# Kernel tuning notes

Hardware: AMD Instinct MI355X
Metric: run time of the kernel (lower is better)

The kernel has to match this reference:

```python
import jax, jax.numpy as jnp
import numpy as np

NUMERICAL_STABILIZER = 1e-3


def relu_kernel(data, projection_matrix):
    # data: [B,L,H,D], projection_matrix: [M,D] -> [B,L,H,M]
    ratio = 1.0 / jnp.sqrt(jnp.asarray(projection_matrix.shape[0], dtype=data.dtype))
    data_dash = ratio * jnp.einsum('blhd,md->blhm', data, projection_matrix)
    return jax.nn.relu(data_dash) + NUMERICAL_STABILIZER


def favor_causal(query, key, value, projection_matrix):
    # query/key/value: [B,L,H,D]; projection_matrix: [M,D]
    qp = relu_kernel(query, projection_matrix)  # [B,L,H,M]
    kp = relu_kernel(key, projection_matrix)    # [B,L,H,M]
    # move L to scan axis: [L,B,H,*]
    qs = jnp.transpose(qp, (1, 0, 2, 3))
    ks = jnp.transpose(kp, (1, 0, 2, 3))
    vs = jnp.transpose(value, (1, 0, 2, 3))

    B, H, M = qs.shape[1], qs.shape[2], qs.shape[3]
    D = vs.shape[3]
    kv0 = jnp.zeros((B, H, M, D), dtype=qs.dtype)
    ksum0 = jnp.zeros((B, H, M), dtype=qs.dtype)

    def step(carry, inp):
        kv_sum, k_sum = carry
        q_t, k_t, v_t = inp  # [B,H,M], [B,H,M], [B,H,D]
        kv_sum = kv_sum + jnp.einsum('bhm,bhd->bhmd', k_t, v_t)
        k_sum = k_sum + k_t
        num_t = jnp.einsum('bhmd,bhm->bhd', kv_sum, q_t)  # [B,H,D]
        den_t = jnp.einsum('bhm,bhm->bh', q_t, k_sum)     # [B,H]
        return (kv_sum, k_sum), (num_t, den_t)

    _, (num, den) = jax.lax.scan(step, (kv0, ksum0), (qs, ks, vs))
    # num: [L,B,H,D], den: [L,B,H]
    out = num / den[..., None]
    return jnp.transpose(out, (1, 0, 2, 3))  # [B,L,H,D]


def setup_inputs() -> dict:
    key = jax.random.key(0)
    k1, k2, k3, k4 = jax.random.split(key, 4)
    B, L, H, D, M = 2, 4096, 8, 64, 128
    return {
        'query': jax.random.normal(k1, (B, L, H, D), dtype=jnp.float32),
        'key': jax.random.normal(k2, (B, L, H, D), dtype=jnp.float32),
        'value': jax.random.normal(k3, (B, L, H, D), dtype=jnp.float32),
        'projection_matrix': jax.random.normal(k4, (M, D), dtype=jnp.float32),
    }


def reference(query, key, value, projection_matrix):
    return favor_causal(query, key, value, projection_matrix)
```

## Files before the change

### kernel.cpp

```cpp
#include <hip/hip_runtime.h>


#define B_ 2
#define L_ 4096
#define H_ 8
#define D_ 64
#define M_ 128
#define BH_ 16
#define HD_ 512
#define LHD_ (L_*HD_)
#define C_ 64
#define T_ 64
#define RATIO 0.08838834764831845f
#define EPS 1e-3f

#define REC_CS 8320
#define REC_F  8192
#define QF_OFF 8519680
#define N2_OFF 16908288
#define RS_OFF 25296896
#define P_OFF  25427968

#define SWZ64(r,c)  ((r)*64  + ((c) ^ (((r)&7)*8)))
#define SWZ128(r,c) ((r)*128 + ((c) ^ (((r)&15)*8)))

typedef __attribute__((ext_vector_type(8))) short bf16x8;
typedef __attribute__((ext_vector_type(4))) short bf16x4;
typedef __attribute__((ext_vector_type(4))) float f32x4;

__device__ __forceinline__ short f2bf(float f) {
  union { float f; unsigned u; } x; x.f = f;
  unsigned r = (x.u + 0x7fffu + ((x.u >> 16) & 1u)) >> 16;
  return (short)r;
}
__device__ __forceinline__ float bf2f(short s) {
  union { unsigned u; float f; } x; x.u = ((unsigned)(unsigned short)s) << 16;
  return x.f;
}
__device__ __forceinline__ bf16x8 cvt8(float4 a, float4 b) {
  union { bf16x8 v; short s[8]; } u;
  u.s[0]=f2bf(a.x); u.s[1]=f2bf(a.y); u.s[2]=f2bf(a.z); u.s[3]=f2bf(a.w);
  u.s[4]=f2bf(b.x); u.s[5]=f2bf(b.y); u.s[6]=f2bf(b.z); u.s[7]=f2bf(b.w);
  return u.v;
}
#define MFMA(a,b,c) __builtin_amdgcn_mfma_f32_16x16x32_bf16((a),(b),(c),0,0,0)

__global__ __launch_bounds__(256) void k0(
    const float* __restrict__ P, unsigned short* __restrict__ ws)
{
  const int i = (blockIdx.x*256 + threadIdx.x)*4;
  float4 p4 = *(const float4*)(P + i);
  union { bf16x4 v; short s[4]; } u;
  u.s[0]=f2bf(p4.x); u.s[1]=f2bf(p4.y); u.s[2]=f2bf(p4.z); u.s[3]=f2bf(p4.w);
  *(bf16x4*)(ws + P_OFF + i) = u.v;
}

__global__ __launch_bounds__(256) void k1(
    const float* __restrict__ qq, const float* __restrict__ kk,
    const float* __restrict__ vv, unsigned short* __restrict__ ws)
{
  __shared__ short Vt[64*64];
  __shared__ short Kft[128*64];
  __shared__ short KfTM[64*128];

  const int tid = threadIdx.x, bid = blockIdx.x;
  const int bh = bid >> 6, c = bid & 63;
  const int b = bh >> 3, h = bh & 7;
  const int lane = tid & 63, w = tid >> 6, quad = lane >> 4, l15 = lane & 15;
  const size_t gbase = (size_t)b*LHD_ + (size_t)h*D_;
  const int t0 = c*T_;
  const int trow = 16*w + l15;
  const unsigned short* Pb = ws + P_OFF;

  const float* qrow = qq + gbase + (size_t)(t0 + trow)*HD_;
  const float* krow = kk + gbase + (size_t)(t0 + trow)*HD_;
  float4 q4a = *(const float4*)(qrow + quad*8);
  float4 q4b = *(const float4*)(qrow + quad*8 + 4);
  float4 q4c = *(const float4*)(qrow + 32 + quad*8);
  float4 q4d = *(const float4*)(qrow + 32 + quad*8 + 4);
  float4 k4a = *(const float4*)(krow + quad*8);
  float4 k4b = *(const float4*)(krow + quad*8 + 4);
  float4 k4c = *(const float4*)(krow + 32 + quad*8);
  float4 k4d = *(const float4*)(krow + 32 + quad*8 + 4);

  for (int fi = tid; fi < 64*16; fi += 256) {
    int t = fi >> 4, d4 = (fi & 15)*4;
    float4 v4 = *(const float4*)(vv + gbase + (size_t)(t0+t)*HD_ + d4);
    Vt[SWZ64(d4+0, t)] = f2bf(v4.x);
    Vt[SWZ64(d4+1, t)] = f2bf(v4.y);
    Vt[SWZ64(d4+2, t)] = f2bf(v4.z);
    Vt[SWZ64(d4+3, t)] = f2bf(v4.w);
  }

  bf16x8 bq0 = cvt8(q4a, q4b), bq1 = cvt8(q4c, q4d);
  bf16x8 bk0 = cvt8(k4a, k4b), bk1 = cvt8(k4c, k4d);

  unsigned short* qfb = ws + QF_OFF + (size_t)(bh*C_+c)*REC_F;
  unsigned short* csb = ws + (size_t)(bh*C_+c)*REC_CS;

  bf16x4 qreg[8];
  #pragma unroll
  for (int ct = 0; ct < 8; ++ct) {
    bf16x8 ap0 = *(const bf16x8*)(Pb + (ct*16 + l15)*64 + quad*8);
    bf16x8 ap1 = *(const bf16x8*)(Pb + (ct*16 + l15)*64 + 32 + quad*8);
    f32x4 qa = {0.f,0.f,0.f,0.f}, ka = {0.f,0.f,0.f,0.f};
    qa = MFMA(ap0,bq0,qa); qa = MFMA(ap1,bq1,qa);
    ka = MFMA(ap0,bk0,ka); ka = MFMA(ap1,bk1,ka);
    union { bf16x4 v; short s[4]; } pq, pk;
    #pragma unroll
    for (int reg = 0; reg < 4; ++reg) {
      int m = 16*ct + 4*quad + reg;
      short qv = f2bf(fmaxf(qa[reg]*RATIO, 0.f) + EPS);
      short kv = f2bf(fmaxf(ka[reg]*RATIO, 0.f) + EPS);
      pq.s[reg] = qv; pk.s[reg] = kv;
      Kft[SWZ64(m, trow)] = kv;
    }
    qreg[ct] = pq.v;
    *(bf16x4*)(qfb + trow*128 + 16*ct + 4*quad) = pq.v;
    *(bf16x4*)&KfTM[SWZ128(trow, 16*ct + 4*quad)] = pk.v;
  }

  bf16x8 qfr[4];
  {
    const int src_lo = (2*(quad & 1))*16 + l15;
    #pragma unroll
    for (int ks2 = 0; ks2 < 4; ++ks2) {
      union { bf16x4 v; long long l; } a0, a1;
      a0.v = qreg[2*ks2]; a1.v = qreg[2*ks2+1];
      long long loA = __shfl(a0.l, src_lo, 64);
      long long hiA = __shfl(a0.l, src_lo + 16, 64);
      long long loB = __shfl(a1.l, src_lo, 64);
      long long hiB = __shfl(a1.l, src_lo + 16, 64);
      union { bf16x8 v8; long long l[2]; } r;
      r.l[0] = (quad < 2) ? loA : loB;
      r.l[1] = (quad < 2) ? hiA : hiB;
      qfr[ks2] = r.v8;
    }
  }
  __syncthreads();

  if (tid < 128) {
    float s = 0.f;
    #pragma unroll
    for (int i = 0; i < 8; ++i) {
      bf16x8 r = *(const bf16x8*)&Kft[SWZ64(tid, 8*i)];
      #pragma unroll
      for (int j = 0; j < 8; ++j) s += bf2f(r[j]);
    }
    csb[64*128 + tid] = (unsigned short)f2bf(s);
  }

  {
    bf16x8 av0 = *(const bf16x8*)&Vt[SWZ64(trow, 8*quad)];
    bf16x8 av1 = *(const bf16x8*)&Vt[SWZ64(trow, 32 + 8*quad)];
    #pragma unroll
    for (int mt = 0; mt < 8; ++mt) {
      bf16x8 b0 = *(const bf16x8*)&Kft[SWZ64(16*mt + l15, 8*quad)];
      bf16x8 b1 = *(const bf16x8*)&Kft[SWZ64(16*mt + l15, 32 + 8*quad)];
      f32x4 acc = {0.f,0.f,0.f,0.f};
      acc = MFMA(b0, av0, acc);
      acc = MFMA(b1, av1, acc);
      union { bf16x4 v; short s[4]; } pc;
      #pragma unroll
      for (int reg = 0; reg < 4; ++reg) pc.s[reg] = f2bf(acc[reg]);
      *(bf16x4*)(csb + trow*128 + 16*mt + 4*quad) = pc.v;
    }
  }

  f32x4 sacc[4];
  #pragma unroll
  for (int jt = 0; jt < 4; ++jt) { f32x4 z = {0.f,0.f,0.f,0.f}; sacc[jt] = z; }
  #pragma unroll
  for (int ks2 = 0; ks2 < 4; ++ks2) {
    #pragma unroll
    for (int jt = 0; jt < 4; ++jt) {
      bf16x8 bb = *(const bf16x8*)&KfTM[SWZ128(16*jt + l15, 32*ks2 + 8*quad)];
      sacc[jt] = MFMA(qfr[ks2], bb, sacc[jt]);
    }
  }
  __syncthreads();

  short* Sm = Kft;
  float rs[4] = {0.f,0.f,0.f,0.f};
  #pragma unroll
  for (int jt = 0; jt < 4; ++jt)
    #pragma unroll
    for (int reg = 0; reg < 4; ++reg) {
      int row = 16*w + 4*quad + reg;
      int j = l15 + 16*jt;
      float val = (j <= row) ? sacc[jt][reg] : 0.f;
      rs[reg] += val;
      Sm[SWZ64(row, j)] = f2bf(val);
    }
  #pragma unroll
  for (int reg = 0; reg < 4; ++reg) {
    rs[reg] += __shfl_xor(rs[reg], 1);
    rs[reg] += __shfl_xor(rs[reg], 2);
    rs[reg] += __shfl_xor(rs[reg], 4);
    rs[reg] += __shfl_xor(rs[reg], 8);
  }
  float* rsg = (float*)(ws + RS_OFF);
  if (l15 < 4) {
    float v = (l15==0) ? rs[0] : (l15==1) ? rs[1] : (l15==2) ? rs[2] : rs[3];
    rsg[bh*L_ + t0 + 16*w + 4*quad + l15] = v;
  }

  float* n2 = (float*)(ws + N2_OFF);
  f32x4 nacc[4];
  #pragma unroll
  for (int ct = 0; ct < 4; ++ct) { f32x4 z = {0.f,0.f,0.f,0.f}; nacc[ct] = z; }
  #pragma unroll
  for (int kss = 0; kss < 2; ++kss) {
    bf16x8 sb = *(const bf16x8*)&Sm[SWZ64(trow, 32*kss + 8*quad)];
    #pragma unroll
    for (int ct = 0; ct < 4; ++ct) {
      bf16x8 a = *(const bf16x8*)&Vt[SWZ64(16*ct + l15, 32*kss + 8*quad)];
      nacc[ct] = MFMA(a, sb, nacc[ct]);
    }
  }
  const int tg = t0 + trow;
  #pragma unroll
  for (int ct = 0; ct < 4; ++ct) {
    float4 o;
    o.x = nacc[ct][0]; o.y = nacc[ct][1]; o.z = nacc[ct][2]; o.w = nacc[ct][3];
    *(float4*)(n2 + gbase + (size_t)tg*HD_ + 16*ct + 4*quad) = o;
  }
}

__global__ __launch_bounds__(64) void k2(unsigned short* __restrict__ ws)
{
  const int gid = blockIdx.x*64 + threadIdx.x;
  const int bh = gid / 2080, e = (gid % 2080)*4;
  unsigned short* base = ws + (size_t)bh*C_*REC_CS + e;
  bf16x4 v[64];
  #pragma unroll
  for (int c2 = 0; c2 < 64; ++c2) v[c2] = *(const bf16x4*)(base + (size_t)c2*REC_CS);
  float run[4] = {0.f,0.f,0.f,0.f};
  #pragma unroll
  for (int c2 = 0; c2 < 64; ++c2) {
    union { bf16x4 v; short s[4]; } wv;
    #pragma unroll
    for (int j = 0; j < 4; ++j) { wv.s[j] = f2bf(run[j]); run[j] += bf2f(v[c2][j]); }
    *(bf16x4*)(base + (size_t)c2*REC_CS) = wv.v;
  }
}

__global__ __launch_bounds__(256) void k3(
    const unsigned short* __restrict__ ws, float* __restrict__ out)
{
  __shared__ short csL[64*128];
  __shared__ float ks_lds[128];

  const int tid = threadIdx.x, bid = blockIdx.x;
  const int bh = bid >> 6, c = bid & 63;
  const int b = bh >> 3, h = bh & 7;
  const int lane = tid & 63, w = tid >> 6, quad = lane >> 4, l15 = lane & 15;
  const size_t gbase = (size_t)b*LHD_ + (size_t)h*D_;
  const int t0 = c*T_;
  const unsigned short* csb = ws + (size_t)(bh*C_+c)*REC_CS;
  const unsigned short* qfb = ws + QF_OFF + (size_t)(bh*C_+c)*REC_F;
  const float* n2 = (const float*)(ws + N2_OFF);
  const float* rsg = (const float*)(ws + RS_OFF);
  const int trow = 16*w + l15;
  const int tg = t0 + trow;

  for (int i = tid; i < 1024; i += 256) {
    int row = i >> 4, cb = (i & 15)*8;
    *(bf16x8*)&csL[SWZ128(row, cb)] = *(const bf16x8*)(csb + i*8);
  }
  if (tid < 128) ks_lds[tid] = bf2f((short)csb[64*128 + tid]);

  float4 nv[4];
  #pragma unroll
  for (int ct = 0; ct < 4; ++ct)
    nv[ct] = *(const float4*)(n2 + gbase + (size_t)tg*HD_ + 16*ct + 4*quad);
  float rsv = rsg[bh*L_ + tg];
  bf16x8 qfB[4];
  #pragma unroll
  for (int ks2 = 0; ks2 < 4; ++ks2)
    qfB[ks2] = *(const bf16x8*)(qfb + trow*128 + ks2*32 + quad*8);

  __syncthreads();

  float dp = 0.f;
  #pragma unroll
  for (int ks2 = 0; ks2 < 4; ++ks2)
    #pragma unroll
    for (int j = 0; j < 8; ++j) dp += bf2f(qfB[ks2][j]) * ks_lds[ks2*32 + quad*8 + j];
  dp += __shfl_xor(dp, 16);
  dp += __shfl_xor(dp, 32);
  float inv = 1.f / (dp + rsv);

  f32x4 nacc[4];
  #pragma unroll
  for (int ct = 0; ct < 4; ++ct) { f32x4 z = {0.f,0.f,0.f,0.f}; nacc[ct] = z; }
  #pragma unroll
  for (int ks2 = 0; ks2 < 4; ++ks2) {
    #pragma unroll
    for (int ct = 0; ct < 4; ++ct) {
      bf16x8 a = *(const bf16x8*)&csL[SWZ128(16*ct + l15, 32*ks2 + 8*quad)];
      nacc[ct] = MFMA(a, qfB[ks2], nacc[ct]);
    }
  }
  #pragma unroll
  for (int ct = 0; ct < 4; ++ct) {
    float4 o;
    o.x = (nacc[ct][0] + nv[ct].x) * inv;
    o.y = (nacc[ct][1] + nv[ct].y) * inv;
    o.z = (nacc[ct][2] + nv[ct].z) * inv;
    o.w = (nacc[ct][3] + nv[ct].w) * inv;
    *(float4*)(out + gbase + (size_t)tg*HD_ + 16*ct + 4*quad) = o;
  }
}

extern "C" void kernel_launch(void* const* d_in, const int* in_sizes, int n_in,
                              void* d_out, int out_size, void* d_ws, size_t ws_size,
                              hipStream_t stream) {
  const float* q = (const float*)d_in[0];
  const float* k = (const float*)d_in[1];
  const float* v = (const float*)d_in[2];
  const float* P = (const float*)d_in[3];
  float* out = (float*)d_out;
  unsigned short* ws = (unsigned short*)d_ws;

  k0<<<dim3(8),      dim3(256), 0, stream>>>(P, ws);
  k1<<<dim3(BH_*C_), dim3(256), 0, stream>>>(q, k, v, ws);
  k2<<<dim3(520),    dim3(64),  0, stream>>>(ws);
  k3<<<dim3(BH_*C_), dim3(256), 0, stream>>>(ws, out);
}
```

Measured before the change: 126.7 us.

## Fuse chunk-local, prefix-scan and output kernels into one cooperative kernel

After: 128.4 us. About the same (+1.3%).

```diff
diff --git a/kernel.cpp b/kernel.cpp
--- a/kernel.cpp
+++ b/kernel.cpp
@@ -1,4 +1,7 @@
 #include <hip/hip_runtime.h>
+#include <hip/hip_cooperative_groups.h>
+
+namespace cg = cooperative_groups;
 
 
 #define B_ 2
@@ -55,6 +58,232 @@
   *(bf16x4*)(ws + P_OFF + i) = u.v;
 }
 
+__global__ __launch_bounds__(256, 4) void kf(
+    const float* __restrict__ qq, const float* __restrict__ kk,
+    const float* __restrict__ vv, unsigned short* __restrict__ ws,
+    float* __restrict__ out)
+{
+  __shared__ short Vt[64*64];
+  __shared__ short Kft[128*64];
+  __shared__ short KfTM[64*128];
+
+  const int tid = threadIdx.x, bid = blockIdx.x;
+  const int bh = bid >> 6, c = bid & 63;
+  const int b = bh >> 3, h = bh & 7;
+  const int lane = tid & 63, w = tid >> 6, quad = lane >> 4, l15 = lane & 15;
+  const size_t gbase = (size_t)b*LHD_ + (size_t)h*D_;
+  const int t0 = c*T_;
+  const int trow = 16*w + l15;
+  const unsigned short* Pb = ws + P_OFF;
+
+  const float* qrow = qq + gbase + (size_t)(t0 + trow)*HD_;
+  const float* krow = kk + gbase + (size_t)(t0 + trow)*HD_;
+  float4 q4a = *(const float4*)(qrow + quad*8);
+  float4 q4b = *(const float4*)(qrow + quad*8 + 4);
+  float4 q4c = *(const float4*)(qrow + 32 + quad*8);
+  float4 q4d = *(const float4*)(qrow + 32 + quad*8 + 4);
+  float4 k4a = *(const float4*)(krow + quad*8);
+  float4 k4b = *(const float4*)(krow + quad*8 + 4);
+  float4 k4c = *(const float4*)(krow + 32 + quad*8);
+  float4 k4d = *(const float4*)(krow + 32 + quad*8 + 4);
+
+  for (int fi = tid; fi < 64*16; fi += 256) {
+    int t = fi >> 4, d4 = (fi & 15)*4;
+    float4 v4 = *(const float4*)(vv + gbase + (size_t)(t0+t)*HD_ + d4);
+    Vt[SWZ64(d4+0, t)] = f2bf(v4.x);
+    Vt[SWZ64(d4+1, t)] = f2bf(v4.y);
+    Vt[SWZ64(d4+2, t)] = f2bf(v4.z);
+    Vt[SWZ64(d4+3, t)] = f2bf(v4.w);
+  }
+
+  bf16x8 bq0 = cvt8(q4a, q4b), bq1 = cvt8(q4c, q4d);
+  bf16x8 bk0 = cvt8(k4a, k4b), bk1 = cvt8(k4c, k4d);
+
+  unsigned short* csb = ws + (size_t)(bh*C_+c)*REC_CS;
+
+  bf16x4 qreg[8];
+  #pragma unroll
+  for (int ct = 0; ct < 8; ++ct) {
+    bf16x8 ap0 = *(const bf16x8*)(Pb + (ct*16 + l15)*64 + quad*8);
+    bf16x8 ap1 = *(const bf16x8*)(Pb + (ct*16 + l15)*64 + 32 + quad*8);
+    f32x4 qa = {0.f,0.f,0.f,0.f}, ka = {0.f,0.f,0.f,0.f};
+    qa = MFMA(ap0,bq0,qa); qa = MFMA(ap1,bq1,qa);
+    ka = MFMA(ap0,bk0,ka); ka = MFMA(ap1,bk1,ka);
+    union { bf16x4 v; short s[4]; } pq, pk;
+    #pragma unroll
+    for (int reg = 0; reg < 4; ++reg) {
+      int m = 16*ct + 4*quad + reg;
+      short qv = f2bf(fmaxf(qa[reg]*RATIO, 0.f) + EPS);
+      short kv = f2bf(fmaxf(ka[reg]*RATIO, 0.f) + EPS);
+      pq.s[reg] = qv; pk.s[reg] = kv;
+      Kft[SWZ64(m, trow)] = kv;
+    }
+    qreg[ct] = pq.v;
+    *(bf16x4*)&KfTM[SWZ128(trow, 16*ct + 4*quad)] = pk.v;
+  }
+
+  bf16x8 qfr[4];
+  {
+    const int src_lo = (2*(quad & 1))*16 + l15;
+    #pragma unroll
+    for (int ks2 = 0; ks2 < 4; ++ks2) {
+      union { bf16x4 v; long long l; } a0, a1;
+      a0.v = qreg[2*ks2]; a1.v = qreg[2*ks2+1];
+      long long loA = __shfl(a0.l, src_lo, 64);
+      long long hiA = __shfl(a0.l, src_lo + 16, 64);
+      long long loB = __shfl(a1.l, src_lo, 64);
+      long long hiB = __shfl(a1.l, src_lo + 16, 64);
+      union { bf16x8 v8; long long l[2]; } r;
+      r.l[0] = (quad < 2) ? loA : loB;
+      r.l[1] = (quad < 2) ? hiA : hiB;
+      qfr[ks2] = r.v8;
+    }
+  }
+  __syncthreads();
+
+  if (tid < 128) {
+    float s = 0.f;
+    #pragma unroll
+    for (int i = 0; i < 8; ++i) {
+      bf16x8 r = *(const bf16x8*)&Kft[SWZ64(tid, 8*i)];
+      #pragma unroll
+      for (int j = 0; j < 8; ++j) s += bf2f(r[j]);
+    }
+    csb[64*128 + tid] = (unsigned short)f2bf(s);
+  }
+
+  {
+    bf16x8 av0 = *(const bf16x8*)&Vt[SWZ64(trow, 8*quad)];
+    bf16x8 av1 = *(const bf16x8*)&Vt[SWZ64(trow, 32 + 8*quad)];
+    #pragma unroll
+    for (int mt = 0; mt < 8; ++mt) {
+      bf16x8 b0 = *(const bf16x8*)&Kft[SWZ64(16*mt + l15, 8*quad)];
+      bf16x8 b1 = *(const bf16x8*)&Kft[SWZ64(16*mt + l15, 32 + 8*quad)];
+      f32x4 acc = {0.f,0.f,0.f,0.f};
+      acc = MFMA(b0, av0, acc);
+      acc = MFMA(b1, av1, acc);
+      union { bf16x4 v; short s[4]; } pc;
+      #pragma unroll
+      for (int reg = 0; reg < 4; ++reg) pc.s[reg] = f2bf(acc[reg]);
+      *(bf16x4*)(csb + trow*128 + 16*mt + 4*quad) = pc.v;
+    }
+  }
+
+  f32x4 sacc[4];
+  #pragma unroll
+  for (int jt = 0; jt < 4; ++jt) { f32x4 z = {0.f,0.f,0.f,0.f}; sacc[jt] = z; }
+  #pragma unroll
+  for (int ks2 = 0; ks2 < 4; ++ks2) {
+    #pragma unroll
+    for (int jt = 0; jt < 4; ++jt) {
+      bf16x8 bb = *(const bf16x8*)&KfTM[SWZ128(16*jt + l15, 32*ks2 + 8*quad)];
+      sacc[jt] = MFMA(qfr[ks2], bb, sacc[jt]);
+    }
+  }
+  __syncthreads();
+
+  short* Sm = Kft;
+  float rs[4] = {0.f,0.f,0.f,0.f};
+  #pragma unroll
+  for (int jt = 0; jt < 4; ++jt)
+    #pragma unroll
+    for (int reg = 0; reg < 4; ++reg) {
+      int row = 16*w + 4*quad + reg;
+      int j = l15 + 16*jt;
+      float val = (j <= row) ? sacc[jt][reg] : 0.f;
+      rs[reg] += val;
+      Sm[SWZ64(row, j)] = f2bf(val);
+    }
+  #pragma unroll
+  for (int reg = 0; reg < 4; ++reg) {
+    rs[reg] += __shfl_xor(rs[reg], 1);
+    rs[reg] += __shfl_xor(rs[reg], 2);
+    rs[reg] += __shfl_xor(rs[reg], 4);
+    rs[reg] += __shfl_xor(rs[reg], 8);
+  }
+  float rsv_ = (l15 < 4) ? ((l15==0)?rs[0]:(l15==1)?rs[1]:(l15==2)?rs[2]:rs[3]) : 0.f;
+  float rsv = __shfl(rsv_, ((l15 >> 2) << 4) + (l15 & 3), 64);
+
+  f32x4 nacc[4];
+  #pragma unroll
+  for (int ct = 0; ct < 4; ++ct) { f32x4 z = {0.f,0.f,0.f,0.f}; nacc[ct] = z; }
+  #pragma unroll
+  for (int kss = 0; kss < 2; ++kss) {
+    bf16x8 sb = *(const bf16x8*)&Sm[SWZ64(trow, 32*kss + 8*quad)];
+    #pragma unroll
+    for (int ct = 0; ct < 4; ++ct) {
+      bf16x8 a = *(const bf16x8*)&Vt[SWZ64(16*ct + l15, 32*kss + 8*quad)];
+      nacc[ct] = MFMA(a, sb, nacc[ct]);
+    }
+  }
+
+  cg::this_grid().sync();
+
+  if (bid < 130) {
+    const int gid = bid*256 + tid;
+    const int pbh = gid / 2080, e = (gid % 2080)*4;
+    unsigned short* base = ws + (size_t)pbh*C_*REC_CS + e;
+    float run[4] = {0.f,0.f,0.f,0.f};
+    #pragma unroll 1
+    for (int batch = 0; batch < 8; ++batch) {
+      bf16x4 pv[8];
+      #pragma unroll
+      for (int u = 0; u < 8; ++u)
+        pv[u] = *(const bf16x4*)(base + (size_t)(batch*8+u)*REC_CS);
+      #pragma unroll
+      for (int u = 0; u < 8; ++u) {
+        union { bf16x4 v; short s[4]; } wv;
+        #pragma unroll
+        for (int j = 0; j < 4; ++j) { wv.s[j] = f2bf(run[j]); run[j] += bf2f(pv[u][j]); }
+        *(bf16x4*)(base + (size_t)(batch*8+u)*REC_CS) = wv.v;
+      }
+    }
+  }
+
+  cg::this_grid().sync();
+
+  short* csL = KfTM;
+  float* ksL = (float*)Vt;
+
+  for (int i = tid; i < 1024; i += 256) {
+    int row = i >> 4, cb = (i & 15)*8;
+    *(bf16x8*)&csL[SWZ128(row, cb)] = *(const bf16x8*)(csb + i*8);
+  }
+  if (tid < 128) ksL[tid] = bf2f((short)csb[64*128 + tid]);
+  __syncthreads();
+
+  float dp = 0.f;
+  #pragma unroll
+  for (int ks2 = 0; ks2 < 4; ++ks2)
+    #pragma unroll
+    for (int j = 0; j < 8; ++j) dp += bf2f(qfr[ks2][j]) * ksL[ks2*32 + quad*8 + j];
+  dp += __shfl_xor(dp, 16);
+  dp += __shfl_xor(dp, 32);
+  float inv = 1.f / (dp + rsv);
+
+  f32x4 n1[4];
+  #pragma unroll
+  for (int ct = 0; ct < 4; ++ct) { f32x4 z = {0.f,0.f,0.f,0.f}; n1[ct] = z; }
+  #pragma unroll
+  for (int ks2 = 0; ks2 < 4; ++ks2) {
+    #pragma unroll
+    for (int ct = 0; ct < 4; ++ct) {
+      bf16x8 a = *(const bf16x8*)&csL[SWZ128(16*ct + l15, 32*ks2 + 8*quad)];
+      n1[ct] = MFMA(a, qfr[ks2], n1[ct]);
+    }
+  }
+  const int tg = t0 + trow;
+  #pragma unroll
+  for (int ct = 0; ct < 4; ++ct) {
+    float4 o;
+    o.x = (n1[ct][0] + nacc[ct][0]) * inv;
+    o.y = (n1[ct][1] + nacc[ct][1]) * inv;
+    o.z = (n1[ct][2] + nacc[ct][2]) * inv;
+    o.w = (n1[ct][3] + nacc[ct][3]) * inv;
+    *(float4*)(out + gbase + (size_t)tg*HD_ + 16*ct + 4*quad) = o;
+  }
+}
+
 __global__ __launch_bounds__(256) void k1(
     const float* __restrict__ qq, const float* __restrict__ kk,
     const float* __restrict__ vv, unsigned short* __restrict__ ws)
@@ -323,7 +552,24 @@
   float* out = (float*)d_out;
   unsigned short* ws = (unsigned short*)d_ws;
 
-  k0<<<dim3(8),      dim3(256), 0, stream>>>(P, ws);
+  static int coop_ok = -1;
+  if (coop_ok < 0) {
+    int nb = 0, cus = 0;
+    hipError_t e1 = hipOccupancyMaxActiveBlocksPerMultiprocessor(&nb, kf, 256, 0);
+    hipError_t e2 = hipDeviceGetAttribute(&cus, hipDeviceAttributeMultiprocessorCount, 0);
+    coop_ok = (e1 == hipSuccess && e2 == hipSuccess && nb * cus >= BH_*C_) ? 1 : 0;
+  }
+
+  k0<<<dim3(8), dim3(256), 0, stream>>>(P, ws);
+
+  if (coop_ok) {
+    void* args[] = { (void*)&q, (void*)&k, (void*)&v, (void*)&ws, (void*)&out };
+    hipError_t e = hipLaunchCooperativeKernel(kf, dim3(BH_*C_), dim3(256),
+                                              args, 0, stream);
+    if (e == hipSuccess) return;
+    coop_ok = 0;
+  }
+
   k1<<<dim3(BH_*C_), dim3(256), 0, stream>>>(q, k, v, ws);
   k2<<<dim3(520),    dim3(64),  0, stream>>>(ws);
   k3<<<dim3(BH_*C_), dim3(256), 0, stream>>>(ws, out);
```

## Recompute query features in k3 instead of storing, and vectorize LDS transposes

Applied to the files above, without the earlier changes.

After: 131.0 us. +3.3%, slower.

```diff
diff --git a/kernel.cpp b/kernel.cpp
--- a/kernel.cpp
+++ b/kernel.cpp
@@ -15,8 +15,6 @@
 #define EPS 1e-3f
 
 #define REC_CS 8320
-#define REC_F  8192
-#define QF_OFF 8519680
 #define N2_OFF 16908288
 #define RS_OFF 25296896
 #define P_OFF  25427968
@@ -83,19 +81,29 @@
   float4 k4c = *(const float4*)(krow + 32 + quad*8);
   float4 k4d = *(const float4*)(krow + 32 + quad*8 + 4);
 
-  for (int fi = tid; fi < 64*16; fi += 256) {
-    int t = fi >> 4, d4 = (fi & 15)*4;
-    float4 v4 = *(const float4*)(vv + gbase + (size_t)(t0+t)*HD_ + d4);
-    Vt[SWZ64(d4+0, t)] = f2bf(v4.x);
-    Vt[SWZ64(d4+1, t)] = f2bf(v4.y);
-    Vt[SWZ64(d4+2, t)] = f2bf(v4.z);
-    Vt[SWZ64(d4+3, t)] = f2bf(v4.w);
+  {
+    const int d4 = (tid & 15)*4, t4 = (tid >> 4)*4;
+    const float* vb = vv + gbase + (size_t)(t0 + t4)*HD_ + d4;
+    float4 va0 = *(const float4*)(vb);
+    float4 va1 = *(const float4*)(vb + HD_);
+    float4 va2 = *(const float4*)(vb + 2*HD_);
+    float4 va3 = *(const float4*)(vb + 3*HD_);
+    const float* p0 = (const float*)&va0;
+    const float* p1 = (const float*)&va1;
+    const float* p2 = (const float*)&va2;
+    const float* p3 = (const float*)&va3;
+    #pragma unroll
+    for (int r = 0; r < 4; ++r) {
+      union { bf16x4 v; short s[4]; } pv;
+      pv.s[0] = f2bf(p0[r]); pv.s[1] = f2bf(p1[r]);
+      pv.s[2] = f2bf(p2[r]); pv.s[3] = f2bf(p3[r]);
+      *(bf16x4*)&Vt[SWZ64(d4 + r, t4)] = pv.v;
+    }
   }
 
   bf16x8 bq0 = cvt8(q4a, q4b), bq1 = cvt8(q4c, q4d);
   bf16x8 bk0 = cvt8(k4a, k4b), bk1 = cvt8(k4c, k4d);
 
-  unsigned short* qfb = ws + QF_OFF + (size_t)(bh*C_+c)*REC_F;
   unsigned short* csb = ws + (size_t)(bh*C_+c)*REC_CS;
 
   bf16x4 qreg[8];
@@ -103,21 +111,20 @@
   for (int ct = 0; ct < 8; ++ct) {
     bf16x8 ap0 = *(const bf16x8*)(Pb + (ct*16 + l15)*64 + quad*8);
     bf16x8 ap1 = *(const bf16x8*)(Pb + (ct*16 + l15)*64 + 32 + quad*8);
-    f32x4 qa = {0.f,0.f,0.f,0.f}, ka = {0.f,0.f,0.f,0.f};
-    qa = MFMA(ap0,bq0,qa); qa = MFMA(ap1,bq1,qa);
-    ka = MFMA(ap0,bk0,ka); ka = MFMA(ap1,bk1,ka);
-    union { bf16x4 v; short s[4]; } pq, pk;
+    f32x4 qa = {0.f,0.f,0.f,0.f}, kas = {0.f,0.f,0.f,0.f}, kan = {0.f,0.f,0.f,0.f};
+    qa  = MFMA(ap0,bq0,qa);  qa  = MFMA(ap1,bq1,qa);
+    kas = MFMA(ap0,bk0,kas); kas = MFMA(ap1,bk1,kas);
+    kan = MFMA(bk0,ap0,kan); kan = MFMA(bk1,ap1,kan);
+    union { bf16x4 v; short s[4]; } pq, pks, pkn;
     #pragma unroll
     for (int reg = 0; reg < 4; ++reg) {
-      int m = 16*ct + 4*quad + reg;
-      short qv = f2bf(fmaxf(qa[reg]*RATIO, 0.f) + EPS);
-      short kv = f2bf(fmaxf(ka[reg]*RATIO, 0.f) + EPS);
-      pq.s[reg] = qv; pk.s[reg] = kv;
-      Kft[SWZ64(m, trow)] = kv;
+      pq.s[reg]  = f2bf(fmaxf(qa[reg] *RATIO, 0.f) + EPS);
+      pks.s[reg] = f2bf(fmaxf(kas[reg]*RATIO, 0.f) + EPS);
+      pkn.s[reg] = f2bf(fmaxf(kan[reg]*RATIO, 0.f) + EPS);
     }
     qreg[ct] = pq.v;
-    *(bf16x4*)(qfb + trow*128 + 16*ct + 4*quad) = pq.v;
-    *(bf16x4*)&KfTM[SWZ128(trow, 16*ct + 4*quad)] = pk.v;
+    *(bf16x4*)&KfTM[SWZ128(trow, 16*ct + 4*quad)] = pks.v;
+    *(bf16x4*)&Kft[SWZ64(l15 + 16*ct, 16*w + 4*quad)] = pkn.v;
   }
 
   bf16x8 qfr[4];
@@ -246,7 +253,8 @@
 }
 
 __global__ __launch_bounds__(256) void k3(
-    const unsigned short* __restrict__ ws, float* __restrict__ out)
+    const float* __restrict__ qq, const unsigned short* __restrict__ ws,
+    float* __restrict__ out)
 {
   __shared__ short csL[64*128];
   __shared__ float ks_lds[128];
@@ -258,12 +266,18 @@
   const size_t gbase = (size_t)b*LHD_ + (size_t)h*D_;
   const int t0 = c*T_;
   const unsigned short* csb = ws + (size_t)(bh*C_+c)*REC_CS;
-  const unsigned short* qfb = ws + QF_OFF + (size_t)(bh*C_+c)*REC_F;
+  const unsigned short* Pb = ws + P_OFF;
   const float* n2 = (const float*)(ws + N2_OFF);
   const float* rsg = (const float*)(ws + RS_OFF);
   const int trow = 16*w + l15;
   const int tg = t0 + trow;
 
+  const float* qrow = qq + gbase + (size_t)tg*HD_;
+  float4 q4a = *(const float4*)(qrow + quad*8);
+  float4 q4b = *(const float4*)(qrow + quad*8 + 4);
+  float4 q4c = *(const float4*)(qrow + 32 + quad*8);
+  float4 q4d = *(const float4*)(qrow + 32 + quad*8 + 4);
+
   for (int i = tid; i < 1024; i += 256) {
     int row = i >> 4, cb = (i & 15)*8;
     *(bf16x8*)&csL[SWZ128(row, cb)] = *(const bf16x8*)(csb + i*8);
@@ -275,18 +289,45 @@
   for (int ct = 0; ct < 4; ++ct)
     nv[ct] = *(const float4*)(n2 + gbase + (size_t)tg*HD_ + 16*ct + 4*quad);
   float rsv = rsg[bh*L_ + tg];
-  bf16x8 qfB[4];
+
+  bf16x8 bq0 = cvt8(q4a, q4b), bq1 = cvt8(q4c, q4d);
+  bf16x4 qreg[8];
+  #pragma unroll
+  for (int ct = 0; ct < 8; ++ct) {
+    bf16x8 ap0 = *(const bf16x8*)(Pb + (ct*16 + l15)*64 + quad*8);
+    bf16x8 ap1 = *(const bf16x8*)(Pb + (ct*16 + l15)*64 + 32 + quad*8);
+    f32x4 qa = {0.f,0.f,0.f,0.f};
+    qa = MFMA(ap0,bq0,qa); qa = MFMA(ap1,bq1,qa);
+    union { bf16x4 v; short s[4]; } pq;
+    #pragma unroll
+    for (int reg = 0; reg < 4; ++reg)
+      pq.s[reg] = f2bf(fmaxf(qa[reg]*RATIO, 0.f) + EPS);
+    qreg[ct] = pq.v;
+  }
+  bf16x8 qfr[4];
+  {
+    const int src_lo = (2*(quad & 1))*16 + l15;
+    #pragma unroll
+    for (int ks2 = 0; ks2 < 4; ++ks2) {
+      union { bf16x4 v; long long l; } a0, a1;
+      a0.v = qreg[2*ks2]; a1.v = qreg[2*ks2+1];
+      long long loA = __shfl(a0.l, src_lo, 64);
+      long long hiA = __shfl(a0.l, src_lo + 16, 64);
+      long long loB = __shfl(a1.l, src_lo, 64);
+      long long hiB = __shfl(a1.l, src_lo + 16, 64);
+      union { bf16x8 v8; long long l[2]; } r;
+      r.l[0] = (quad < 2) ? loA : loB;
+      r.l[1] = (quad < 2) ? hiA : hiB;
+      qfr[ks2] = r.v8;
+    }
+  }
+  __syncthreads();
+
+  float dp = 0.f;
   #pragma unroll
   for (int ks2 = 0; ks2 < 4; ++ks2)
-    qfB[ks2] = *(const bf16x8*)(qfb + trow*128 + ks2*32 + quad*8);
-
-  __syncthreads();
-
-  float dp = 0.f;
-  #pragma unroll
-  for (int ks2 = 0; ks2 < 4; ++ks2)
-    #pragma unroll
-    for (int j = 0; j < 8; ++j) dp += bf2f(qfB[ks2][j]) * ks_lds[ks2*32 + quad*8 + j];
+    #pragma unroll
+    for (int j = 0; j < 8; ++j) dp += bf2f(qfr[ks2][j]) * ks_lds[ks2*32 + quad*8 + j];
   dp += __shfl_xor(dp, 16);
   dp += __shfl_xor(dp, 32);
   float inv = 1.f / (dp + rsv);
@@ -299,7 +340,7 @@
     #pragma unroll
     for (int ct = 0; ct < 4; ++ct) {
       bf16x8 a = *(const bf16x8*)&csL[SWZ128(16*ct + l15, 32*ks2 + 8*quad)];
-      nacc[ct] = MFMA(a, qfB[ks2], nacc[ct]);
+      nacc[ct] = MFMA(a, qfr[ks2], nacc[ct]);
     }
   }
   #pragma unroll
@@ -326,5 +367,5 @@
   k0<<<dim3(8),      dim3(256), 0, stream>>>(P, ws);
   k1<<<dim3(BH_*C_), dim3(256), 0, stream>>>(q, k, v, ws);
   k2<<<dim3(520),    dim3(64),  0, stream>>>(ws);
-  k3<<<dim3(BH_*C_), dim3(256), 0, stream>>>(ws, out);
-}
+  k3<<<dim3(BH_*C_), dim3(256), 0, stream>>>(q, ws, out);
+}
```

## Vectorize LDS transposes in k1 and double k2 parallelism

Applied to the files above, without the earlier changes.

New measurement: 128.0 us. No clear change (+1.0%).

```diff
diff --git a/kernel.cpp b/kernel.cpp
--- a/kernel.cpp
+++ b/kernel.cpp
@@ -26,6 +26,7 @@
 
 typedef __attribute__((ext_vector_type(8))) short bf16x8;
 typedef __attribute__((ext_vector_type(4))) short bf16x4;
+typedef __attribute__((ext_vector_type(2))) short bf16x2;
 typedef __attribute__((ext_vector_type(4))) float f32x4;
 
 __device__ __forceinline__ short f2bf(float f) {
@@ -83,13 +84,24 @@
   float4 k4c = *(const float4*)(krow + 32 + quad*8);
   float4 k4d = *(const float4*)(krow + 32 + quad*8 + 4);
 
-  for (int fi = tid; fi < 64*16; fi += 256) {
-    int t = fi >> 4, d4 = (fi & 15)*4;
-    float4 v4 = *(const float4*)(vv + gbase + (size_t)(t0+t)*HD_ + d4);
-    Vt[SWZ64(d4+0, t)] = f2bf(v4.x);
-    Vt[SWZ64(d4+1, t)] = f2bf(v4.y);
-    Vt[SWZ64(d4+2, t)] = f2bf(v4.z);
-    Vt[SWZ64(d4+3, t)] = f2bf(v4.w);
+  {
+    const int d4 = (tid & 15)*4, t4 = (tid >> 4)*4;
+    const float* vb = vv + gbase + (size_t)(t0 + t4)*HD_ + d4;
+    float4 va0 = *(const float4*)(vb);
+    float4 va1 = *(const float4*)(vb + HD_);
+    float4 va2 = *(const float4*)(vb + 2*HD_);
+    float4 va3 = *(const float4*)(vb + 3*HD_);
+    const float* p0 = (const float*)&va0;
+    const float* p1 = (const float*)&va1;
+    const float* p2 = (const float*)&va2;
+    const float* p3 = (const float*)&va3;
+    #pragma unroll
+    for (int r = 0; r < 4; ++r) {
+      union { bf16x4 v; short s[4]; } pv;
+      pv.s[0] = f2bf(p0[r]); pv.s[1] = f2bf(p1[r]);
+      pv.s[2] = f2bf(p2[r]); pv.s[3] = f2bf(p3[r]);
+      *(bf16x4*)&Vt[SWZ64(d4 + r, t4)] = pv.v;
+    }
   }
 
   bf16x8 bq0 = cvt8(q4a, q4b), bq1 = cvt8(q4c, q4d);
@@ -103,21 +115,21 @@
   for (int ct = 0; ct < 8; ++ct) {
     bf16x8 ap0 = *(const bf16x8*)(Pb + (ct*16 + l15)*64 + quad*8);
     bf16x8 ap1 = *(const bf16x8*)(Pb + (ct*16 + l15)*64 + 32 + quad*8);
-    f32x4 qa = {0.f,0.f,0.f,0.f}, ka = {0.f,0.f,0.f,0.f};
-    qa = MFMA(ap0,bq0,qa); qa = MFMA(ap1,bq1,qa);
-    ka = MFMA(ap0,bk0,ka); ka = MFMA(ap1,bk1,ka);
-    union { bf16x4 v; short s[4]; } pq, pk;
+    f32x4 qa = {0.f,0.f,0.f,0.f}, kas = {0.f,0.f,0.f,0.f}, kan = {0.f,0.f,0.f,0.f};
+    qa  = MFMA(ap0,bq0,qa);  qa  = MFMA(ap1,bq1,qa);
+    kas = MFMA(ap0,bk0,kas); kas = MFMA(ap1,bk1,kas);
+    kan = MFMA(bk0,ap0,kan); kan = MFMA(bk1,ap1,kan);
+    union { bf16x4 v; short s[4]; } pq, pks, pkn;
     #pragma unroll
     for (int reg = 0; reg < 4; ++reg) {
-      int m = 16*ct + 4*quad + reg;
-      short qv = f2bf(fmaxf(qa[reg]*RATIO, 0.f) + EPS);
-      short kv = f2bf(fmaxf(ka[reg]*RATIO, 0.f) + EPS);
-      pq.s[reg] = qv; pk.s[reg] = kv;
-      Kft[SWZ64(m, trow)] = kv;
+      pq.s[reg]  = f2bf(fmaxf(qa[reg] *RATIO, 0.f) + EPS);
+      pks.s[reg] = f2bf(fmaxf(kas[reg]*RATIO, 0.f) + EPS);
+      pkn.s[reg] = f2bf(fmaxf(kan[reg]*RATIO, 0.f) + EPS);
     }
     qreg[ct] = pq.v;
     *(bf16x4*)(qfb + trow*128 + 16*ct + 4*quad) = pq.v;
-    *(bf16x4*)&KfTM[SWZ128(trow, 16*ct + 4*quad)] = pk.v;
+    *(bf16x4*)&KfTM[SWZ128(trow, 16*ct + 4*quad)] = pks.v;
+    *(bf16x4*)&Kft[SWZ64(l15 + 16*ct, 16*w + 4*quad)] = pkn.v;
   }
 
   bf16x8 qfr[4];
@@ -230,18 +242,18 @@
 __global__ __launch_bounds__(64) void k2(unsigned short* __restrict__ ws)
 {
   const int gid = blockIdx.x*64 + threadIdx.x;
-  const int bh = gid / 2080, e = (gid % 2080)*4;
+  const int bh = gid / 4160, e = (gid % 4160)*2;
   unsigned short* base = ws + (size_t)bh*C_*REC_CS + e;
-  bf16x4 v[64];
-  #pragma unroll
-  for (int c2 = 0; c2 < 64; ++c2) v[c2] = *(const bf16x4*)(base + (size_t)c2*REC_CS);
-  float run[4] = {0.f,0.f,0.f,0.f};
+  bf16x2 v[64];
+  #pragma unroll
+  for (int c2 = 0; c2 < 64; ++c2) v[c2] = *(const bf16x2*)(base + (size_t)c2*REC_CS);
+  float run[2] = {0.f,0.f};
   #pragma unroll
   for (int c2 = 0; c2 < 64; ++c2) {
-    union { bf16x4 v; short s[4]; } wv;
-    #pragma unroll
-    for (int j = 0; j < 4; ++j) { wv.s[j] = f2bf(run[j]); run[j] += bf2f(v[c2][j]); }
-    *(bf16x4*)(base + (size_t)c2*REC_CS) = wv.v;
+    union { bf16x2 v; short s[2]; } wv;
+    #pragma unroll
+    for (int j = 0; j < 2; ++j) { wv.s[j] = f2bf(run[j]); run[j] += bf2f(v[c2][j]); }
+    *(bf16x2*)(base + (size_t)c2*REC_CS) = wv.v;
   }
 }
 
@@ -325,6 +337,6 @@
 
   k0<<<dim3(8),      dim3(256), 0, stream>>>(P, ws);
   k1<<<dim3(BH_*C_), dim3(256), 0, stream>>>(q, k, v, ws);
-  k2<<<dim3(520),    dim3(64),  0, stream>>>(ws);
+  k2<<<dim3(1040),   dim3(64),  0, stream>>>(ws);
   k3<<<dim3(BH_*C_), dim3(256), 0, stream>>>(ws, out);
 }
```
